# Kernel optimization log

Measured on AMD Instinct MI355X. Metric: run time of the kernel, lower is better.

The kernel has to match this reference:

```python
import jax, jax.numpy as jnp
import numpy as np


def setup_inputs() -> dict:
    key = jax.random.key(0)
    kq, kk, kv = jax.random.split(key, 3)
    b, n, h, d = 1, 8192, 8, 64
    return {
        "query": jax.random.normal(kq, (b, n, h, d), dtype=jnp.float32),
        "key": jax.random.normal(kk, (b, n, h, d), dtype=jnp.float32),
        "value": jax.random.normal(kv, (b, n, h, d), dtype=jnp.float32),
        "ring_size": 4,
    }


def _ring_attention(q, k, v, ring_size):
    # q,k,v: [b, n, h, d]. Emulates the ring: K/V split into ring_size chunks,
    # processed sequentially with online-softmax rescaling (non-causal).
    b, n, h, d = q.shape
    cs = n // ring_size  # chunk_size
    scale = 1.0 / jnp.sqrt(jnp.asarray(d, q.dtype))
    # [ring, b, cs, h, d]
    k_chunks = jnp.moveaxis(k.reshape(b, ring_size, cs, h, d), 1, 0)
    v_chunks = jnp.moveaxis(v.reshape(b, ring_size, cs, h, d), 1, 0)

    out0 = jnp.zeros((b, h, n, d), q.dtype)
    m0 = jnp.full((b, h, n, 1), -jnp.inf, q.dtype)
    s0 = jnp.zeros((b, h, n, 1), q.dtype)

    def step(carry, kv_chunk):
        out, m, s = carry
        kc, vc = kv_chunk  # [b, cs, h, d]
        scores = jnp.einsum("bqhd,bkhd->bhqk", q, kc) * scale  # [b,h,n,cs]
        chunk_max = scores.max(axis=-1, keepdims=True)
        new_max = jnp.maximum(m, chunk_max)
        corr = jnp.exp(m - new_max)  # 0 at first step since m=-inf
        exp_scores = jnp.exp(scores - new_max)
        out = out * corr + jnp.einsum("bhqk,bkhd->bhqd", exp_scores, vc)
        s = s * corr + exp_scores.sum(axis=-1, keepdims=True)
        return (out, new_max, s), None

    (out, _, s), _ = jax.lax.scan(step, (out0, m0, s0), (k_chunks, v_chunks))
    out = out / s
    return jnp.swapaxes(out, 1, 2)  # [b, n, h, d]


def reference(query, key, value, ring_size):
    return _ring_attention(query, key, value, ring_size)
```

## Files before the change

### kernel.cpp

```cpp
#include <hip/hip_runtime.h>
#include <hip/hip_bf16.h>

typedef __attribute__((ext_vector_type(8))) short bf16x8;
typedef __attribute__((ext_vector_type(8))) unsigned short u16x8;
typedef __attribute__((ext_vector_type(16))) float f32x16;
typedef __attribute__((ext_vector_type(4))) unsigned int u32x4;

#define MFMA32(a, b, c) __builtin_amdgcn_mfma_f32_32x32x16_bf16(a, b, c, 0, 0, 0)

constexpr int NSEQ = 8192;
constexpr int NH   = 8;
constexpr int DIM  = 64;
constexpr int KVB  = 64;
constexpr int QB   = 128;
constexpr int NT   = NSEQ / KVB;
constexpr int NTH  = NT / 2;
constexpr int SLAB = KVB * DIM;
constexpr float SCL2 = 0.18033688011112042f;

__device__ __forceinline__ unsigned cvt_pk(float lo, float hi) {
    unsigned r;
    asm("v_cvt_pk_bf16_f32 %0, %1, %2" : "=v"(r) : "v"(lo), "v"(hi));
    return r;
}
__device__ __forceinline__ float exp2f_fast(float x) {
    float r;
    asm("v_exp_f32 %0, %1" : "=v"(r) : "v"(x));
    return r;
}
__device__ __forceinline__ void pl32swap(unsigned& a, unsigned& b) {
    asm("v_permlane32_swap_b32 %0, %1" : "+v"(a), "+v"(b));
}
__device__ __forceinline__ int swz(int row, int col) {
    return row * 64 + ((((col >> 3) ^ row) & 7) << 3) + (col & 7);
}

__global__ __launch_bounds__(256, 4)
void prep_kernel(const float* __restrict__ Kg, const float* __restrict__ Vg,
                 unsigned short* __restrict__ Kws, unsigned short* __restrict__ Vws) {
    __shared__ float Vf[64][65];
    const int tid = threadIdx.x;
    const int bid = blockIdx.x;
    if (bid < 1024) {
        const int h = bid >> 7, t = bid & 127;
        unsigned short* dst = Kws + (size_t)bid * SLAB;
#pragma unroll
        for (int j = 0; j < 2; ++j) {
            const int m = tid * 2 + j;
            const int instr = m >> 6, ln = m & 63;
            const int kh = instr >> 2, kd = instr & 3;
            const int row = t * 64 + kh * 32 + (ln & 31);
            const int col = kd * 16 + (ln >> 5) * 8;
            const float* src = Kg + ((size_t)row * NH + h) * DIM + col;
            float4 a = ((const float4*)src)[0];
            float4 b = ((const float4*)src)[1];
            u32x4 w;
            w[0] = cvt_pk(a.x, a.y); w[1] = cvt_pk(a.z, a.w);
            w[2] = cvt_pk(b.x, b.y); w[3] = cvt_pk(b.z, b.w);
            *(u32x4*)(dst + m * 8) = w;
        }
    } else {
        const int hb = bid - 1024;
        const int h = hb >> 7, t = hb & 127;
        const int key = tid >> 2, dc = (tid & 3) * 16;
        const float* src = Vg + ((size_t)(t * 64 + key) * NH + h) * DIM + dc;
#pragma unroll
        for (int i = 0; i < 4; ++i) {
            float4 a = ((const float4*)src)[i];
            Vf[key][dc + i * 4 + 0] = a.x; Vf[key][dc + i * 4 + 1] = a.y;
            Vf[key][dc + i * 4 + 2] = a.z; Vf[key][dc + i * 4 + 3] = a.w;
        }
        __syncthreads();
        unsigned short* dst = Vws + (size_t)hb * SLAB;
#pragma unroll
        for (int j = 0; j < 2; ++j) {
            const int m = tid * 2 + j;
            const int instr = m >> 6, ln = m & 63;
            const int vh = instr >> 2, ks = instr & 3;
            const int d  = vh * 32 + (ln & 31);
            const int k0 = ks * 16 + (ln >> 5) * 8;
            u32x4 w;
            w[0] = cvt_pk(Vf[k0 + 0][d], Vf[k0 + 1][d]);
            w[1] = cvt_pk(Vf[k0 + 2][d], Vf[k0 + 3][d]);
            w[2] = cvt_pk(Vf[k0 + 4][d], Vf[k0 + 5][d]);
            w[3] = cvt_pk(Vf[k0 + 6][d], Vf[k0 + 7][d]);
            *(u32x4*)(dst + m * 8) = w;
        }
    }
}

__global__ __launch_bounds__(512, 4)
void fa_kernel(const float* __restrict__ Qg, const unsigned short* __restrict__ Kws,
               const unsigned short* __restrict__ Vws, float* __restrict__ Og) {
    __shared__ unsigned short Kb[2][2][SLAB];
    __shared__ unsigned short Vb[2][2][SLAB];

    const int tid  = threadIdx.x;
    const int lane = tid & 63;
    const int wave = tid >> 6;
    const int half = wave >> 2;
    const int qw   = wave & 3;
    const int la31 = lane & 31;
    const int hi   = lane >> 5;
    const int halftid = tid & 255;
    const int head  = blockIdx.x & 7;
    const int qtile = blockIdx.x >> 3;
    const int q     = qtile * QB + qw * 32 + la31;
    const int fragoff = lane * 8;

    bf16x8 qf[4];
#pragma unroll
    for (int kd = 0; kd < 4; ++kd) {
        const float* qp = Qg + ((size_t)q * NH + head) * DIM + kd * 16 + hi * 8;
        float4 a = ((const float4*)qp)[0];
        float4 b = ((const float4*)qp)[1];
        u32x4 w;
        w[0] = cvt_pk(a.x * SCL2, a.y * SCL2);
        w[1] = cvt_pk(a.z * SCL2, a.w * SCL2);
        w[2] = cvt_pk(b.x * SCL2, b.y * SCL2);
        w[3] = cvt_pk(b.z * SCL2, b.w * SCL2);
        qf[kd] = __builtin_bit_cast(bf16x8, w);
    }

    const unsigned short* ksl = Kws + ((size_t)head * NT + (size_t)half * NTH) * SLAB + halftid * 8;
    const unsigned short* vsl = Vws + ((size_t)head * NT + (size_t)half * NTH) * SLAB + halftid * 8;

    f32x16 oacc[2];
#pragma unroll
    for (int nt = 0; nt < 2; ++nt)
#pragma unroll
        for (int i = 0; i < 16; ++i) oacc[nt][i] = 0.f;
    float m_run = -1e30f, l_run = 0.f;

    u16x8 kr0 = *(const u16x8*)ksl, kr1 = *(const u16x8*)(ksl + 2048);
    u16x8 vr0 = *(const u16x8*)vsl, vr1 = *(const u16x8*)(vsl + 2048);
    ksl += SLAB; vsl += SLAB;

    for (int t = 0; t < NTH; ++t) {
        const int cur = t & 1;
        *(u16x8*)&Kb[half][cur][halftid * 8]        = kr0;
        *(u16x8*)&Kb[half][cur][2048 + halftid * 8] = kr1;
        *(u16x8*)&Vb[half][cur][halftid * 8]        = vr0;
        *(u16x8*)&Vb[half][cur][2048 + halftid * 8] = vr1;
        __syncthreads();
        if (t + 1 < NTH) {
            kr0 = *(const u16x8*)ksl; kr1 = *(const u16x8*)(ksl + 2048);
            vr0 = *(const u16x8*)vsl; vr1 = *(const u16x8*)(vsl + 2048);
            ksl += SLAB; vsl += SLAB;
        }
        const unsigned short* Kbase = &Kb[half][cur][0];
        const unsigned short* Vbase = &Vb[half][cur][0];

        f32x16 s0, s1;
#pragma unroll
        for (int i = 0; i < 16; ++i) { s0[i] = 0.f; s1[i] = 0.f; }
        __builtin_amdgcn_s_setprio(1);
#pragma unroll
        for (int kd = 0; kd < 4; ++kd) {
            bf16x8 k0 = *(const bf16x8*)(Kbase + kd * 512 + fragoff);
            bf16x8 k1 = *(const bf16x8*)(Kbase + (4 + kd) * 512 + fragoff);
            s0 = MFMA32(k0, qf[kd], s0);
            s1 = MFMA32(k1, qf[kd], s1);
        }
        __builtin_amdgcn_s_setprio(0);

        float pmv[16];
#pragma unroll
        for (int i = 0; i < 16; ++i) pmv[i] = fmaxf(s0[i], s1[i]);
#pragma unroll
        for (int st = 8; st >= 1; st >>= 1)
#pragma unroll
            for (int i = 0; i < 8; ++i)
                if (i < st) pmv[i] = fmaxf(pmv[i], pmv[i + st]);
        float pm = pmv[0];
        pm = fmaxf(pm, __shfl_xor(pm, 32));

        if (__any(pm > m_run + 8.f)) {
            float mnew = fmaxf(m_run, pm);
            float corr = exp2f_fast(m_run - mnew);
            m_run = mnew;
            l_run *= corr;
#pragma unroll
            for (int i = 0; i < 16; ++i) { oacc[0][i] *= corr; oacc[1][i] *= corr; }
        }

#pragma unroll
        for (int kb = 0; kb < 2; ++kb) {
            const f32x16& s = kb ? s1 : s0;
            float p[16];
#pragma unroll
            for (int i = 0; i < 16; ++i) p[i] = exp2f_fast(s[i] - m_run);
            float ts[8];
#pragma unroll
            for (int i = 0; i < 8; ++i) ts[i] = p[i] + p[i + 8];
#pragma unroll
            for (int i = 0; i < 4; ++i) ts[i] += ts[i + 4];
            l_run += (ts[0] + ts[1]) + (ts[2] + ts[3]);
            unsigned A[8];
#pragma unroll
            for (int j = 0; j < 8; ++j) A[j] = cvt_pk(p[2 * j], p[2 * j + 1]);
            pl32swap(A[0], A[2]); pl32swap(A[1], A[3]);
            pl32swap(A[4], A[6]); pl32swap(A[5], A[7]);
            u32x4 f0v; f0v[0] = A[0]; f0v[1] = A[1]; f0v[2] = A[2]; f0v[3] = A[3];
            u32x4 f1v; f1v[0] = A[4]; f1v[1] = A[5]; f1v[2] = A[6]; f1v[3] = A[7];
            bf16x8 frag[2] = { __builtin_bit_cast(bf16x8, f0v), __builtin_bit_cast(bf16x8, f1v) };

            __builtin_amdgcn_s_setprio(1);
#pragma unroll
            for (int ksl2 = 0; ksl2 < 2; ++ksl2) {
                const int ksg = kb * 2 + ksl2;
                bf16x8 vf0 = *(const bf16x8*)(Vbase + ksg * 512 + fragoff);
                bf16x8 vf1 = *(const bf16x8*)(Vbase + (4 + ksg) * 512 + fragoff);
                oacc[0] = MFMA32(vf0, frag[ksl2], oacc[0]);
                oacc[1] = MFMA32(vf1, frag[ksl2], oacc[1]);
            }
            __builtin_amdgcn_s_setprio(0);
        }
    }

    __syncthreads();
    float* mrgO  = (float*)&Kb[0][0][0];
    float* mrgML = (float*)&Vb[0][0][0];
    const int idx = qw * 64 + lane;
    if (half) {
#pragma unroll
        for (int i = 0; i < 16; ++i) {
            mrgO[i * 256 + idx]        = oacc[0][i];
            mrgO[(16 + i) * 256 + idx] = oacc[1][i];
        }
        mrgML[idx]       = m_run;
        mrgML[256 + idx] = l_run;
    }
    __syncthreads();
    if (!half) {
        const float m1 = mrgML[idx], l1 = mrgML[256 + idx];
        const float mnew = fmaxf(m_run, m1);
        const float c0 = exp2f_fast(m_run - mnew);
        const float c1 = exp2f_fast(m1 - mnew);
        float lt = l_run * c0 + l1 * c1;
#pragma unroll
        for (int i = 0; i < 16; ++i) {
            oacc[0][i] = oacc[0][i] * c0 + mrgO[i * 256 + idx] * c1;
            oacc[1][i] = oacc[1][i] * c0 + mrgO[(16 + i) * 256 + idx] * c1;
        }
        const float l_tot = lt + __shfl_xor(lt, 32);
        const float inv = __builtin_amdgcn_rcpf(l_tot);
        float* obase = Og + ((size_t)q * NH + head) * DIM;
#pragma unroll
        for (int nt = 0; nt < 2; ++nt)
#pragma unroll
            for (int rq = 0; rq < 4; ++rq) {
                float4 o;
                o.x = oacc[nt][rq * 4 + 0] * inv;
                o.y = oacc[nt][rq * 4 + 1] * inv;
                o.z = oacc[nt][rq * 4 + 2] * inv;
                o.w = oacc[nt][rq * 4 + 3] * inv;
                *(float4*)(obase + nt * 32 + rq * 8 + hi * 4) = o;
            }
    }
}

__global__ __launch_bounds__(256, 2)
void fb_kernel(const float* __restrict__ Qg, const float* __restrict__ Kg,
               const float* __restrict__ Vg, float* __restrict__ Og) {
    __shared__ unsigned short Kl[KVB][DIM];
    __shared__ unsigned short Vt[DIM][KVB];
    unsigned short* Kbase = &Kl[0][0];
    unsigned short* Vbase = &Vt[0][0];
    const int tid  = threadIdx.x;
    const int lane = tid & 63;
    const int wave = tid >> 6;
    const int la31 = lane & 31;
    const int hi   = lane >> 5;
    const int head  = blockIdx.x & 7;
    const int qtile = blockIdx.x >> 3;
    const int q     = qtile * QB + wave * 32 + la31;
    bf16x8 qf[4];
#pragma unroll
    for (int kd = 0; kd < 4; ++kd) {
        const float* qp = Qg + ((size_t)q * NH + head) * DIM + kd * 16 + hi * 8;
        float4 a = ((const float4*)qp)[0];
        float4 b = ((const float4*)qp)[1];
        u32x4 w;
        w[0] = cvt_pk(a.x * SCL2, a.y * SCL2);
        w[1] = cvt_pk(a.z * SCL2, a.w * SCL2);
        w[2] = cvt_pk(b.x * SCL2, b.y * SCL2);
        w[3] = cvt_pk(b.z * SCL2, b.w * SCL2);
        qf[kd] = __builtin_bit_cast(bf16x8, w);
    }
    const int ksrow = tid & 63;
    const int kscol = (tid >> 6) * 16;
    const int vpair = tid & 31;
    const int vcg   = tid >> 5;
    const float* kptr  = Kg + ((size_t)ksrow * NH + head) * DIM + kscol;
    const float* vptr0 = Vg + ((size_t)(2 * vpair) * NH + head) * DIM + vcg * 8;
    const float* vptr1 = vptr0 + NH * DIM;
    constexpr size_t STRIDE = (size_t)KVB * NH * DIM;
    const int kIdx0 = swz(ksrow, kscol);
    const int kIdx1 = swz(ksrow, kscol + 8);
    f32x16 oacc[2];
#pragma unroll
    for (int nt = 0; nt < 2; ++nt)
#pragma unroll
        for (int i = 0; i < 16; ++i) oacc[nt][i] = 0.f;
    float m_run = -1e30f, l_run = 0.f;
    float4 kr0 = ((const float4*)kptr)[0], kr1 = ((const float4*)kptr)[1];
    float4 kr2 = ((const float4*)kptr)[2], kr3 = ((const float4*)kptr)[3];
    float4 va0 = ((const float4*)vptr0)[0], va1 = ((const float4*)vptr0)[1];
    float4 vb0 = ((const float4*)vptr1)[0], vb1 = ((const float4*)vptr1)[1];
    kptr += STRIDE; vptr0 += STRIDE; vptr1 += STRIDE;
    for (int t = 0; t < NT; ++t) {
        __syncthreads();
        {
            u32x4 w;
            w[0] = cvt_pk(kr0.x, kr0.y); w[1] = cvt_pk(kr0.z, kr0.w);
            w[2] = cvt_pk(kr1.x, kr1.y); w[3] = cvt_pk(kr1.z, kr1.w);
            *(u32x4*)(Kbase + kIdx0) = w;
            w[0] = cvt_pk(kr2.x, kr2.y); w[1] = cvt_pk(kr2.z, kr2.w);
            w[2] = cvt_pk(kr3.x, kr3.y); w[3] = cvt_pk(kr3.z, kr3.w);
            *(u32x4*)(Kbase + kIdx1) = w;
        }
        {
            *(unsigned*)(Vbase + swz(vcg * 8 + 0, 2 * vpair)) = cvt_pk(va0.x, vb0.x);
            *(unsigned*)(Vbase + swz(vcg * 8 + 1, 2 * vpair)) = cvt_pk(va0.y, vb0.y);
            *(unsigned*)(Vbase + swz(vcg * 8 + 2, 2 * vpair)) = cvt_pk(va0.z, vb0.z);
            *(unsigned*)(Vbase + swz(vcg * 8 + 3, 2 * vpair)) = cvt_pk(va0.w, vb0.w);
            *(unsigned*)(Vbase + swz(vcg * 8 + 4, 2 * vpair)) = cvt_pk(va1.x, vb1.x);
            *(unsigned*)(Vbase + swz(vcg * 8 + 5, 2 * vpair)) = cvt_pk(va1.y, vb1.y);
            *(unsigned*)(Vbase + swz(vcg * 8 + 6, 2 * vpair)) = cvt_pk(va1.z, vb1.z);
            *(unsigned*)(Vbase + swz(vcg * 8 + 7, 2 * vpair)) = cvt_pk(va1.w, vb1.w);
        }
        __syncthreads();
        if (t + 1 < NT) {
            kr0 = ((const float4*)kptr)[0]; kr1 = ((const float4*)kptr)[1];
            kr2 = ((const float4*)kptr)[2]; kr3 = ((const float4*)kptr)[3];
            va0 = ((const float4*)vptr0)[0]; va1 = ((const float4*)vptr0)[1];
            vb0 = ((const float4*)vptr1)[0]; vb1 = ((const float4*)vptr1)[1];
            kptr += STRIDE; vptr0 += STRIDE; vptr1 += STRIDE;
        }
        f32x16 s0, s1;
#pragma unroll
        for (int i = 0; i < 16; ++i) { s0[i] = 0.f; s1[i] = 0.f; }
        __builtin_amdgcn_s_setprio(1);
#pragma unroll
        for (int kd = 0; kd < 4; ++kd) {
            bf16x8 k0 = *(const bf16x8*)(Kbase + swz(la31, kd * 16 + hi * 8));
            bf16x8 k1 = *(const bf16x8*)(Kbase + swz(32 + la31, kd * 16 + hi * 8));
            s0 = MFMA32(k0, qf[kd], s0);
            s1 = MFMA32(k1, qf[kd], s1);
        }
        __builtin_amdgcn_s_setprio(0);
        float pmv[16];
#pragma unroll
        for (int i = 0; i < 16; ++i) pmv[i] = fmaxf(s0[i], s1[i]);
#pragma unroll
        for (int st = 8; st >= 1; st >>= 1)
#pragma unroll
            for (int i = 0; i < 8; ++i)
                if (i < st) pmv[i] = fmaxf(pmv[i], pmv[i + st]);
        float pm = pmv[0];
        pm = fmaxf(pm, __shfl_xor(pm, 32));
        if (__any(pm > m_run + 8.f)) {
            float mnew = fmaxf(m_run, pm);
            float corr = exp2f_fast(m_run - mnew);
            m_run = mnew;
            l_run *= corr;
#pragma unroll
            for (int i = 0; i < 16; ++i) { oacc[0][i] *= corr; oacc[1][i] *= corr; }
        }
#pragma unroll
        for (int kb = 0; kb < 2; ++kb) {
            const f32x16& s = kb ? s1 : s0;
            float p[16];
#pragma unroll
            for (int i = 0; i < 16; ++i) p[i] = exp2f_fast(s[i] - m_run);
            float ts[8];
#pragma unroll
            for (int i = 0; i < 8; ++i) ts[i] = p[i] + p[i + 8];
#pragma unroll
            for (int i = 0; i < 4; ++i) ts[i] += ts[i + 4];
            l_run += (ts[0] + ts[1]) + (ts[2] + ts[3]);
            unsigned A[8];
#pragma unroll
            for (int j = 0; j < 8; ++j) A[j] = cvt_pk(p[2 * j], p[2 * j + 1]);
            pl32swap(A[0], A[2]); pl32swap(A[1], A[3]);
            pl32swap(A[4], A[6]); pl32swap(A[5], A[7]);
            u32x4 f0v; f0v[0] = A[0]; f0v[1] = A[1]; f0v[2] = A[2]; f0v[3] = A[3];
            u32x4 f1v; f1v[0] = A[4]; f1v[1] = A[5]; f1v[2] = A[6]; f1v[3] = A[7];
            bf16x8 frag[2] = { __builtin_bit_cast(bf16x8, f0v), __builtin_bit_cast(bf16x8, f1v) };
            __builtin_amdgcn_s_setprio(1);
#pragma unroll
            for (int ksl = 0; ksl < 2; ++ksl) {
                const int ksg = kb * 2 + ksl;
                bf16x8 vf0 = *(const bf16x8*)(Vbase + swz(la31, ksg * 16 + hi * 8));
                bf16x8 vf1 = *(const bf16x8*)(Vbase + swz(32 + la31, ksg * 16 + hi * 8));
                oacc[0] = MFMA32(vf0, frag[ksl], oacc[0]);
                oacc[1] = MFMA32(vf1, frag[ksl], oacc[1]);
            }
            __builtin_amdgcn_s_setprio(0);
        }
    }
    {
        float l_tot = l_run + __shfl_xor(l_run, 32);
        float inv = __builtin_amdgcn_rcpf(l_tot);
        float* obase = Og + ((size_t)q * NH + head) * DIM;
#pragma unroll
        for (int nt = 0; nt < 2; ++nt)
#pragma unroll
            for (int rq = 0; rq < 4; ++rq) {
                float4 o;
                o.x = oacc[nt][rq * 4 + 0] * inv;
                o.y = oacc[nt][rq * 4 + 1] * inv;
                o.z = oacc[nt][rq * 4 + 2] * inv;
                o.w = oacc[nt][rq * 4 + 3] * inv;
                *(float4*)(obase + nt * 32 + rq * 8 + hi * 4) = o;
            }
    }
}

extern "C" void kernel_launch(void* const* d_in, const int* in_sizes, int n_in,
                              void* d_out, int out_size, void* d_ws, size_t ws_size,
                              hipStream_t stream) {
    const float* q = (const float*)d_in[0];
    const float* k = (const float*)d_in[1];
    const float* v = (const float*)d_in[2];
    float* out = (float*)d_out;
    constexpr size_t KV_WS = 2ull * NH * NT * SLAB * sizeof(unsigned short);
    if (ws_size >= KV_WS) {
        unsigned short* Kws = (unsigned short*)d_ws;
        unsigned short* Vws = Kws + (size_t)NH * NT * SLAB;
        hipLaunchKernelGGL(prep_kernel, dim3(2048), dim3(256), 0, stream, k, v, Kws, Vws);
        hipLaunchKernelGGL(fa_kernel, dim3(512), dim3(512), 0, stream, q, Kws, Vws, out);
    } else {
        hipLaunchKernelGGL(fb_kernel, dim3(512), dim3(256), 0, stream, q, k, v, out);
    }
}
```

Before: 203.2 us.

## Give each wave two 32-row query groups to reuse K/V fragments

Each wave now processes two 32-row query groups, so every K and V fragment read from LDS feeds twice as many MFMAs. The block shrinks to 256 threads (4 waves, two per KV half) while still covering 128 queries, and each thread loads twice as much K/V into shared memory. Register pressure roughly doubles per wave (two output accumulators and two sets of score tiles), so launch bounds drop to 2 blocks per CU. This trades occupancy and latency hiding for less LDS traffic per MFMA.

Measured after the change: 182.9 us. 1.11x faster.

```diff
diff --git a/kernel.cpp b/kernel.cpp
--- a/kernel.cpp
+++ b/kernel.cpp
@@ -12,10 +12,10 @@
 constexpr int NH   = 8;
 constexpr int DIM  = 64;
 constexpr int KVB  = 64;
-constexpr int QB   = 128;
 constexpr int NT   = NSEQ / KVB;
 constexpr int NTH  = NT / 2;
 constexpr int SLAB = KVB * DIM;
+constexpr int QB   = 256;
 constexpr float SCL2 = 0.18033688011112042f;
 
 __device__ __forceinline__ unsigned cvt_pk(float lo, float hi) {
@@ -89,174 +89,216 @@
     }
 }
 
-__global__ __launch_bounds__(512, 4)
+__global__ __launch_bounds__(512, 2)
 void fa_kernel(const float* __restrict__ Qg, const unsigned short* __restrict__ Kws,
                const unsigned short* __restrict__ Vws, float* __restrict__ Og) {
-    __shared__ unsigned short Kb[2][2][SLAB];
-    __shared__ unsigned short Vb[2][2][SLAB];
+    __shared__ unsigned short KVb[2][2][2][SLAB];
+    __shared__ float mrgML[2][2][256];
 
     const int tid  = threadIdx.x;
     const int lane = tid & 63;
     const int wave = tid >> 6;
     const int half = wave >> 2;
-    const int qw   = wave & 3;
+    const int qw   = wave & 1;
+    const int qw2  = (wave >> 1) & 1;
     const int la31 = lane & 31;
     const int hi   = lane >> 5;
     const int halftid = tid & 255;
     const int head  = blockIdx.x & 7;
     const int qtile = blockIdx.x >> 3;
-    const int q     = qtile * QB + qw * 32 + la31;
+    const int qwv = wave & 3;
+    const int qv = wave & 3;
+    const int qbase = qtile * 128 + (qv & 1) * 64;
     const int fragoff = lane * 8;
 
-    bf16x8 qf[4];
-#pragma unroll
-    for (int kd = 0; kd < 4; ++kd) {
-        const float* qp = Qg + ((size_t)q * NH + head) * DIM + kd * 16 + hi * 8;
-        float4 a = ((const float4*)qp)[0];
-        float4 b = ((const float4*)qp)[1];
-        u32x4 w;
-        w[0] = cvt_pk(a.x * SCL2, a.y * SCL2);
-        w[1] = cvt_pk(a.z * SCL2, a.w * SCL2);
-        w[2] = cvt_pk(b.x * SCL2, b.y * SCL2);
-        w[3] = cvt_pk(b.z * SCL2, b.w * SCL2);
-        qf[kd] = __builtin_bit_cast(bf16x8, w);
-    }
-
-    const unsigned short* ksl = Kws + ((size_t)head * NT + (size_t)half * NTH) * SLAB + halftid * 8;
-    const unsigned short* vsl = Vws + ((size_t)head * NT + (size_t)half * NTH) * SLAB + halftid * 8;
-
-    f32x16 oacc[2];
-#pragma unroll
-    for (int nt = 0; nt < 2; ++nt)
-#pragma unroll
-        for (int i = 0; i < 16; ++i) oacc[nt][i] = 0.f;
-    float m_run = -1e30f, l_run = 0.f;
-
-    u16x8 kr0 = *(const u16x8*)ksl, kr1 = *(const u16x8*)(ksl + 2048);
-    u16x8 vr0 = *(const u16x8*)vsl, vr1 = *(const u16x8*)(vsl + 2048);
+    const int half_f  = wave >> 1;
+    const int qv_f    = wave & 1;
+    const int qbase_f = qtile * 128 + qv_f * 64;
+    const int halftid_f = tid & 127;
+
+    bf16x8 qf[2][4];
+#pragma unroll
+    for (int g = 0; g < 2; ++g)
+#pragma unroll
+        for (int kd = 0; kd < 4; ++kd) {
+            const float* qp = Qg + ((size_t)(qbase_f + g * 32 + la31) * NH + head) * DIM + kd * 16 + hi * 8;
+            float4 a = ((const float4*)qp)[0];
+            float4 b = ((const float4*)qp)[1];
+            u32x4 w;
+            w[0] = cvt_pk(a.x * SCL2, a.y * SCL2);
+            w[1] = cvt_pk(a.z * SCL2, a.w * SCL2);
+            w[2] = cvt_pk(b.x * SCL2, b.y * SCL2);
+            w[3] = cvt_pk(b.z * SCL2, b.w * SCL2);
+            qf[g][kd] = __builtin_bit_cast(bf16x8, w);
+        }
+
+    const unsigned short* ksl = Kws + ((size_t)head * NT + (size_t)half_f * NTH) * SLAB + halftid_f * 8;
+    const unsigned short* vsl = Vws + ((size_t)head * NT + (size_t)half_f * NTH) * SLAB + halftid_f * 8;
+
+    f32x16 oacc[2][2];
+#pragma unroll
+    for (int g = 0; g < 2; ++g)
+#pragma unroll
+        for (int nt = 0; nt < 2; ++nt)
+#pragma unroll
+            for (int i = 0; i < 16; ++i) oacc[g][nt][i] = 0.f;
+    float m_run[2] = {-1e30f, -1e30f}, l_run[2] = {0.f, 0.f};
+
+    u16x8 kr0 = *(const u16x8*)ksl,          kr1 = *(const u16x8*)(ksl + 1024);
+    u16x8 kr2 = *(const u16x8*)(ksl + 2048), kr3 = *(const u16x8*)(ksl + 3072);
+    u16x8 vr0 = *(const u16x8*)vsl,          vr1 = *(const u16x8*)(vsl + 1024);
+    u16x8 vr2 = *(const u16x8*)(vsl + 2048), vr3 = *(const u16x8*)(vsl + 3072);
     ksl += SLAB; vsl += SLAB;
 
     for (int t = 0; t < NTH; ++t) {
         const int cur = t & 1;
-        *(u16x8*)&Kb[half][cur][halftid * 8]        = kr0;
-        *(u16x8*)&Kb[half][cur][2048 + halftid * 8] = kr1;
-        *(u16x8*)&Vb[half][cur][halftid * 8]        = vr0;
-        *(u16x8*)&Vb[half][cur][2048 + halftid * 8] = vr1;
+        unsigned short* kw = &KVb[0][half_f][cur][0];
+        unsigned short* vw = &KVb[1][half_f][cur][0];
+        *(u16x8*)(kw + halftid_f * 8)        = kr0;
+        *(u16x8*)(kw + 1024 + halftid_f * 8) = kr1;
+        *(u16x8*)(kw + 2048 + halftid_f * 8) = kr2;
+        *(u16x8*)(kw + 3072 + halftid_f * 8) = kr3;
+        *(u16x8*)(vw + halftid_f * 8)        = vr0;
+        *(u16x8*)(vw + 1024 + halftid_f * 8) = vr1;
+        *(u16x8*)(vw + 2048 + halftid_f * 8) = vr2;
+        *(u16x8*)(vw + 3072 + halftid_f * 8) = vr3;
         __syncthreads();
         if (t + 1 < NTH) {
-            kr0 = *(const u16x8*)ksl; kr1 = *(const u16x8*)(ksl + 2048);
-            vr0 = *(const u16x8*)vsl; vr1 = *(const u16x8*)(vsl + 2048);
+            kr0 = *(const u16x8*)ksl;          kr1 = *(const u16x8*)(ksl + 1024);
+            kr2 = *(const u16x8*)(ksl + 2048); kr3 = *(const u16x8*)(ksl + 3072);
+            vr0 = *(const u16x8*)vsl;          vr1 = *(const u16x8*)(vsl + 1024);
+            vr2 = *(const u16x8*)(vsl + 2048); vr3 = *(const u16x8*)(vsl + 3072);
             ksl += SLAB; vsl += SLAB;
         }
-        const unsigned short* Kbase = &Kb[half][cur][0];
-        const unsigned short* Vbase = &Vb[half][cur][0];
-
-        f32x16 s0, s1;
-#pragma unroll
-        for (int i = 0; i < 16; ++i) { s0[i] = 0.f; s1[i] = 0.f; }
+        const unsigned short* Kbase = &KVb[0][half_f][cur][0];
+        const unsigned short* Vbase = &KVb[1][half_f][cur][0];
+
+        f32x16 s00, s01, s10, s11;
+#pragma unroll
+        for (int i = 0; i < 16; ++i) { s00[i] = 0.f; s01[i] = 0.f; s10[i] = 0.f; s11[i] = 0.f; }
         __builtin_amdgcn_s_setprio(1);
 #pragma unroll
         for (int kd = 0; kd < 4; ++kd) {
             bf16x8 k0 = *(const bf16x8*)(Kbase + kd * 512 + fragoff);
             bf16x8 k1 = *(const bf16x8*)(Kbase + (4 + kd) * 512 + fragoff);
-            s0 = MFMA32(k0, qf[kd], s0);
-            s1 = MFMA32(k1, qf[kd], s1);
+            s00 = MFMA32(k0, qf[0][kd], s00);
+            s01 = MFMA32(k1, qf[0][kd], s01);
+            s10 = MFMA32(k0, qf[1][kd], s10);
+            s11 = MFMA32(k1, qf[1][kd], s11);
         }
         __builtin_amdgcn_s_setprio(0);
 
-        float pmv[16];
-#pragma unroll
-        for (int i = 0; i < 16; ++i) pmv[i] = fmaxf(s0[i], s1[i]);
-#pragma unroll
-        for (int st = 8; st >= 1; st >>= 1)
-#pragma unroll
-            for (int i = 0; i < 8; ++i)
-                if (i < st) pmv[i] = fmaxf(pmv[i], pmv[i + st]);
-        float pm = pmv[0];
-        pm = fmaxf(pm, __shfl_xor(pm, 32));
-
-        if (__any(pm > m_run + 8.f)) {
-            float mnew = fmaxf(m_run, pm);
-            float corr = exp2f_fast(m_run - mnew);
-            m_run = mnew;
-            l_run *= corr;
-#pragma unroll
-            for (int i = 0; i < 16; ++i) { oacc[0][i] *= corr; oacc[1][i] *= corr; }
+#pragma unroll
+        for (int g = 0; g < 2; ++g) {
+            const f32x16& a = g ? s10 : s00;
+            const f32x16& b = g ? s11 : s01;
+            float pmv[16];
+#pragma unroll
+            for (int i = 0; i < 16; ++i) pmv[i] = fmaxf(a[i], b[i]);
+#pragma unroll
+            for (int st = 8; st >= 1; st >>= 1)
+#pragma unroll
+                for (int i = 0; i < 8; ++i)
+                    if (i < st) pmv[i] = fmaxf(pmv[i], pmv[i + st]);
+            float pm = pmv[0];
+            pm = fmaxf(pm, __shfl_xor(pm, 32));
+            if (__any(pm > m_run[g] + 8.f)) {
+                float mnew = fmaxf(m_run[g], pm);
+                float corr = exp2f_fast(m_run[g] - mnew);
+                m_run[g] = mnew;
+                l_run[g] *= corr;
+#pragma unroll
+                for (int i = 0; i < 16; ++i) { oacc[g][0][i] *= corr; oacc[g][1][i] *= corr; }
+            }
         }
 
 #pragma unroll
         for (int kb = 0; kb < 2; ++kb) {
-            const f32x16& s = kb ? s1 : s0;
-            float p[16];
-#pragma unroll
-            for (int i = 0; i < 16; ++i) p[i] = exp2f_fast(s[i] - m_run);
-            float ts[8];
-#pragma unroll
-            for (int i = 0; i < 8; ++i) ts[i] = p[i] + p[i + 8];
-#pragma unroll
-            for (int i = 0; i < 4; ++i) ts[i] += ts[i + 4];
-            l_run += (ts[0] + ts[1]) + (ts[2] + ts[3]);
-            unsigned A[8];
-#pragma unroll
-            for (int j = 0; j < 8; ++j) A[j] = cvt_pk(p[2 * j], p[2 * j + 1]);
-            pl32swap(A[0], A[2]); pl32swap(A[1], A[3]);
-            pl32swap(A[4], A[6]); pl32swap(A[5], A[7]);
-            u32x4 f0v; f0v[0] = A[0]; f0v[1] = A[1]; f0v[2] = A[2]; f0v[3] = A[3];
-            u32x4 f1v; f1v[0] = A[4]; f1v[1] = A[5]; f1v[2] = A[6]; f1v[3] = A[7];
-            bf16x8 frag[2] = { __builtin_bit_cast(bf16x8, f0v), __builtin_bit_cast(bf16x8, f1v) };
-
+            bf16x8 frg[2][2];
+#pragma unroll
+            for (int g = 0; g < 2; ++g) {
+                const f32x16& s = g ? (kb ? s11 : s10) : (kb ? s01 : s00);
+                float p[16];
+#pragma unroll
+                for (int i = 0; i < 16; ++i) p[i] = exp2f_fast(s[i] - m_run[g]);
+                float ts[8];
+#pragma unroll
+                for (int i = 0; i < 8; ++i) ts[i] = p[i] + p[i + 8];
+#pragma unroll
+                for (int i = 0; i < 4; ++i) ts[i] += ts[i + 4];
+                l_run[g] += (ts[0] + ts[1]) + (ts[2] + ts[3]);
+                unsigned A[8];
+#pragma unroll
+                for (int j = 0; j < 8; ++j) A[j] = cvt_pk(p[2 * j], p[2 * j + 1]);
+                pl32swap(A[0], A[2]); pl32swap(A[1], A[3]);
+                pl32swap(A[4], A[6]); pl32swap(A[5], A[7]);
+                u32x4 f0v; f0v[0] = A[0]; f0v[1] = A[1]; f0v[2] = A[2]; f0v[3] = A[3];
+                u32x4 f1v; f1v[0] = A[4]; f1v[1] = A[5]; f1v[2] = A[6]; f1v[3] = A[7];
+                frg[g][0] = __builtin_bit_cast(bf16x8, f0v);
+                frg[g][1] = __builtin_bit_cast(bf16x8, f1v);
+            }
             __builtin_amdgcn_s_setprio(1);
 #pragma unroll
-            for (int ksl2 = 0; ksl2 < 2; ++ksl2) {
-                const int ksg = kb * 2 + ksl2;
+            for (int ks2 = 0; ks2 < 2; ++ks2) {
+                const int ksg = kb * 2 + ks2;
                 bf16x8 vf0 = *(const bf16x8*)(Vbase + ksg * 512 + fragoff);
                 bf16x8 vf1 = *(const bf16x8*)(Vbase + (4 + ksg) * 512 + fragoff);
-                oacc[0] = MFMA32(vf0, frag[ksl2], oacc[0]);
-                oacc[1] = MFMA32(vf1, frag[ksl2], oacc[1]);
+                oacc[0][0] = MFMA32(vf0, frg[0][ks2], oacc[0][0]);
+                oacc[0][1] = MFMA32(vf1, frg[0][ks2], oacc[0][1]);
+                oacc[1][0] = MFMA32(vf0, frg[1][ks2], oacc[1][0]);
+                oacc[1][1] = MFMA32(vf1, frg[1][ks2], oacc[1][1]);
             }
             __builtin_amdgcn_s_setprio(0);
         }
     }
 
     __syncthreads();
-    float* mrgO  = (float*)&Kb[0][0][0];
-    float* mrgML = (float*)&Vb[0][0][0];
-    const int idx = qw * 64 + lane;
-    if (half) {
-#pragma unroll
-        for (int i = 0; i < 16; ++i) {
-            mrgO[i * 256 + idx]        = oacc[0][i];
-            mrgO[(16 + i) * 256 + idx] = oacc[1][i];
-        }
-        mrgML[idx]       = m_run;
-        mrgML[256 + idx] = l_run;
+    float* mrgO = (float*)&KVb[0][0][0][0];
+    const int row0 = qv_f * 64;
+    if (half_f) {
+#pragma unroll
+        for (int g = 0; g < 2; ++g) {
+            const int row = row0 + g * 32 + la31;
+#pragma unroll
+            for (int nt = 0; nt < 2; ++nt)
+#pragma unroll
+                for (int i = 0; i < 16; ++i)
+                    mrgO[hi * 4096 + (nt * 16 + i) * 128 + row] = oacc[g][nt][i];
+            mrgML[g][0][qv_f * 64 + lane] = m_run[g];
+            mrgML[g][1][qv_f * 64 + lane] = l_run[g];
+        }
     }
     __syncthreads();
-    if (!half) {
-        const float m1 = mrgML[idx], l1 = mrgML[256 + idx];
-        const float mnew = fmaxf(m_run, m1);
-        const float c0 = exp2f_fast(m_run - mnew);
-        const float c1 = exp2f_fast(m1 - mnew);
-        float lt = l_run * c0 + l1 * c1;
-#pragma unroll
-        for (int i = 0; i < 16; ++i) {
-            oacc[0][i] = oacc[0][i] * c0 + mrgO[i * 256 + idx] * c1;
-            oacc[1][i] = oacc[1][i] * c0 + mrgO[(16 + i) * 256 + idx] * c1;
-        }
-        const float l_tot = lt + __shfl_xor(lt, 32);
-        const float inv = __builtin_amdgcn_rcpf(l_tot);
-        float* obase = Og + ((size_t)q * NH + head) * DIM;
-#pragma unroll
-        for (int nt = 0; nt < 2; ++nt)
-#pragma unroll
-            for (int rq = 0; rq < 4; ++rq) {
-                float4 o;
-                o.x = oacc[nt][rq * 4 + 0] * inv;
-                o.y = oacc[nt][rq * 4 + 1] * inv;
-                o.z = oacc[nt][rq * 4 + 2] * inv;
-                o.w = oacc[nt][rq * 4 + 3] * inv;
-                *(float4*)(obase + nt * 32 + rq * 8 + hi * 4) = o;
-            }
+    if (!half_f) {
+#pragma unroll
+        for (int g = 0; g < 2; ++g) {
+            const int row = row0 + g * 32 + la31;
+            const float m1 = mrgML[g][0][qv_f * 64 + lane];
+            const float l1 = mrgML[g][1][qv_f * 64 + lane];
+            const float mnew = fmaxf(m_run[g], m1);
+            const float c0 = exp2f_fast(m_run[g] - mnew);
+            const float c1 = exp2f_fast(m1 - mnew);
+            float lt = l_run[g] * c0 + l1 * c1;
+#pragma unroll
+            for (int nt = 0; nt < 2; ++nt)
+#pragma unroll
+                for (int i = 0; i < 16; ++i)
+                    oacc[g][nt][i] = oacc[g][nt][i] * c0 + mrgO[hi * 4096 + (nt * 16 + i) * 128 + row] * c1;
+            const float l_tot = lt + __shfl_xor(lt, 32);
+            const float inv = __builtin_amdgcn_rcpf(l_tot);
+            float* obase = Og + ((size_t)(qtile * 128 + row) * NH + head) * DIM;
+#pragma unroll
+            for (int nt = 0; nt < 2; ++nt)
+#pragma unroll
+                for (int rq = 0; rq < 4; ++rq) {
+                    float4 o;
+                    o.x = oacc[g][nt][rq * 4 + 0] * inv;
+                    o.y = oacc[g][nt][rq * 4 + 1] * inv;
+                    o.z = oacc[g][nt][rq * 4 + 2] * inv;
+                    o.w = oacc[g][nt][rq * 4 + 3] * inv;
+                    *(float4*)(obase + nt * 32 + rq * 8 + hi * 4) = o;
+                }
+        }
     }
 }
 
@@ -274,7 +316,7 @@
     const int hi   = lane >> 5;
     const int head  = blockIdx.x & 7;
     const int qtile = blockIdx.x >> 3;
-    const int q     = qtile * QB + wave * 32 + la31;
+    const int q     = qtile * 128 + wave * 32 + la31;
     bf16x8 qf[4];
 #pragma unroll
     for (int kd = 0; kd < 4; ++kd) {
@@ -430,7 +472,7 @@
         unsigned short* Kws = (unsigned short*)d_ws;
         unsigned short* Vws = Kws + (size_t)NH * NT * SLAB;
         hipLaunchKernelGGL(prep_kernel, dim3(2048), dim3(256), 0, stream, k, v, Kws, Vws);
-        hipLaunchKernelGGL(fa_kernel, dim3(512), dim3(512), 0, stream, q, Kws, Vws, out);
+        hipLaunchKernelGGL(fa_kernel, dim3(512), dim3(256), 0, stream, q, Kws, Vws, out);
     } else {
         hipLaunchKernelGGL(fb_kernel, dim3(512), dim3(256), 0, stream, q, k, v, out);
     }
```
